# Kernel optimization log

Hardware: AMD Instinct MI355X
Metric: run time of the kernel (lower is better)

## Reference

```python
import jax, jax.numpy as jnp
import numpy as np

HID = 64
NUM_LAYERS = 4
IN_DIM = 1
OUT_DIM = 1
LN_EPS = 1e-5


def setup_inputs() -> dict:
    key = jax.random.key(0)
    ks = jax.random.split(key, 2 * NUM_LAYERS + 5)
    B, S = 1024, 512
    inp = {"x": jax.random.normal(ks[0], (B, S, IN_DIM), dtype=jnp.float32)}
    # per-layer gate weights, stored as [in+H, 4H] (x @ W + b, equivalent to torch Linear)
    for l in range(NUM_LAYERS):
        in_dim = IN_DIM if l == 0 else HID
        fan_in = in_dim + HID
        bound = 1.0 / np.sqrt(fan_in)
        inp[f"W{l}"] = jax.random.uniform(ks[1 + 2 * l], (fan_in, 4 * HID), jnp.float32, -bound, bound)
        inp[f"b{l}"] = jax.random.uniform(ks[2 + 2 * l], (4 * HID,), jnp.float32, -bound, bound)
    inp["ln_g"] = jnp.ones((HID,), jnp.float32)
    inp["ln_b"] = jnp.zeros((HID,), jnp.float32)
    bo = 1.0 / np.sqrt(HID)
    inp["Wout"] = jax.random.uniform(ks[-2], (HID, OUT_DIM), jnp.float32, -bo, bo)
    inp["bout"] = jax.random.uniform(ks[-1], (OUT_DIM,), jnp.float32, -bo, bo)
    return inp


def _lstm_forward(x, Ws, bs):
    B = x.shape[0]
    h0 = tuple(jnp.zeros((B, HID), x.dtype) for _ in range(NUM_LAYERS))
    c0 = tuple(jnp.zeros((B, HID), x.dtype) for _ in range(NUM_LAYERS))

    def step(carry, xt):
        h, c = carry
        inp = xt
        new_h, new_c = [], []
        for l in range(NUM_LAYERS):
            z = jnp.concatenate([inp, h[l]], axis=-1) @ Ws[l] + bs[l]  # [B, 4H]
            i, f, g, o = jnp.split(z, 4, axis=-1)
            i = jax.nn.sigmoid(i)
            f = jax.nn.sigmoid(f)
            g = jnp.tanh(g)
            o = jax.nn.sigmoid(o)
            c_new = f * c[l] + i * g
            h_new = o * jnp.tanh(c_new)
            new_h.append(h_new)
            new_c.append(c_new)
            inp = h_new
        return (tuple(new_h), tuple(new_c)), new_h[-1]

    xs = jnp.swapaxes(x, 0, 1)  # [S, B, in]
    _, outs = jax.lax.scan(step, (h0, c0), xs)
    return jnp.swapaxes(outs, 0, 1)  # [B, S, H]


def reference(x, W0, b0, W1, b1, W2, b2, W3, b3, ln_g, ln_b, Wout, bout):
    Ws = (W0, W1, W2, W3)
    bs = (b0, b1, b2, b3)
    out = _lstm_forward(x, Ws, bs)  # [B, S, H]
    mu = jnp.mean(out, axis=-1, keepdims=True)
    var = jnp.mean(jnp.square(out - mu), axis=-1, keepdims=True)
    normed = (out - mu) * jax.lax.rsqrt(var + LN_EPS) * ln_g + ln_b
    return normed @ Wout + bout  # [B, S, 1]
```

## Files before the change

### kernel.cpp

```cpp
#include <hip/hip_runtime.h>

#define SEQ   512
#define NTHR  1024
#define NBLK  256

typedef _Float16 f16x8 __attribute__((ext_vector_type(8)));
typedef float    f32x4 __attribute__((ext_vector_type(4)));

#define MFMA(a, b, c) __builtin_amdgcn_mfma_f32_16x16x32_f16((a), (b), (c), 0, 0, 0)

__device__ __forceinline__ float sig_(float x) {
    return __builtin_amdgcn_rcpf(1.0f + __builtin_amdgcn_exp2f(x * -1.4426950408889634f));
}
__device__ __forceinline__ float tanh_(float x) {
    return fmaf(2.0f, __builtin_amdgcn_rcpf(1.0f + __builtin_amdgcn_exp2f(x * -2.8853900817779268f)), -1.0f);
}

__global__ __launch_bounds__(NTHR, 4) void lstm4_pipe16b(
    const float* __restrict__ x,
    const float* __restrict__ W0, const float* __restrict__ B0,
    const float* __restrict__ W1, const float* __restrict__ B1,
    const float* __restrict__ W2, const float* __restrict__ B2,
    const float* __restrict__ W3, const float* __restrict__ B3,
    const float* __restrict__ ln_g, const float* __restrict__ ln_b,
    const float* __restrict__ Wout, const float* __restrict__ bout,
    float* __restrict__ out)
{
    __shared__ __align__(16) _Float16 hbuf[2][4][4][64];
    __shared__ float xall[4][SEQ];
    __shared__ float part[16][4][4][3];
    __shared__ float sconst[2];

    const int tid  = threadIdx.x;
    const int lane = tid & 63;
    const int w    = tid >> 6;
    const int ell  = w >> 2;
    const int om   = w & 3;
    const int lam  = lane >> 4;
    const int bc   = lane & 15;
    const int br   = bc & 3;
    const int k    = bc >> 2;
    const int bb   = blockIdx.x;

    for (int i = tid; i < 4 * SEQ; i += NTHR)
        xall[i >> 9][i & 511] = x[bb * 4 * SEQ + i];
    for (int i = tid; i < 2 * 4 * 4 * 64; i += NTHR)
        ((_Float16*)hbuf)[i] = (_Float16)0.0f;

    if (tid < 64) {
        float a = ln_g[tid] * Wout[tid];
        float b = ln_b[tid] * Wout[tid];
#pragma unroll
        for (int off = 32; off > 0; off >>= 1) {
            a += __shfl_xor(a, off, 64);
            b += __shfl_xor(b, off, 64);
        }
        if (tid == 0) { sconst[0] = a; sconst[1] = b; }
    }

    const float* Wp = (ell == 0) ? W0 : (ell == 1) ? W1 : (ell == 2) ? W2 : W3;
    const float* Bp = (ell == 0) ? B0 : (ell == 1) ? B1 : (ell == 2) ? B2 : B3;

    f16x8 wf[4][4];
    f32x4 biasv[4];
#pragma unroll
    for (int i = 0; i < 4; ++i) {
        const int T  = om * 4 + i;
        const int cA = (bc & 3) * 64 + T * 4 + (bc >> 2);
        if (ell == 0) {
#pragma unroll
            for (int kt = 0; kt < 2; ++kt)
#pragma unroll
                for (int e = 0; e < 8; ++e)
                    wf[i][kt][e] = (_Float16)W0[(1 + kt * 32 + lam * 8 + e) * 256 + cA];
#pragma unroll
            for (int e = 0; e < 8; ++e) { wf[i][2][e] = (_Float16)0.0f; wf[i][3][e] = (_Float16)0.0f; }
            if (lam == 0) wf[i][2][0] = (_Float16)W0[cA];
        } else {
#pragma unroll
            for (int kt = 0; kt < 4; ++kt)
#pragma unroll
                for (int e = 0; e < 8; ++e)
                    wf[i][kt][e] = (_Float16)Wp[(kt * 32 + lam * 8 + e) * 256 + cA];
        }
#pragma unroll
        for (int r = 0; r < 4; ++r)
            biasv[i][r] = Bp[r * 64 + T * 4 + lam];
    }

    const int   mK  = (om * 4 + k) * 4 + lam;
    const float gwK = ln_g[mK] * Wout[mK];
    const int   wrK = br * 128 + (((mK >> 3) ^ br) * 16) + (mK & 7) * 2;

    const int a0 = br * 128 + ((lam)     ^ br) * 16;
    const int a1 = br * 128 + ((4 + lam) ^ br) * 16;

    const bool k1b = (bc & 4) != 0;
    const bool k2b = (bc & 8) != 0;

    float cstK = 0.0f;
    char* const hb = (char*)hbuf;

    __syncthreads();
    const float Sgw = sconst[0];
    const float Sbw = sconst[1] + bout[0];

    for (int tau = 0; tau < SEQ + 3; ++tau) {
        const char* bR = hb + (((tau + 1) & 1) ? 2048 : 0);
        char*       bW = hb + (((tau    ) & 1) ? 2048 : 0);
        const int  t      = tau - ell;
        const bool active = (t >= 0) && (t < SEQ);

        if (active) {
            f16x8 b0, b1, b2, b3;
            if (ell == 0) {
                b0 = *(const f16x8*)(bR + a0);
                b1 = *(const f16x8*)(bR + a1);
                f16x8 xf;
#pragma unroll
                for (int e = 0; e < 8; ++e) xf[e] = (_Float16)0.0f;
                if (lam == 0) xf[0] = (_Float16)xall[br][t];
                b2 = xf; b3 = xf;
            } else {
                const char* bIn   = bR + (ell - 1) * 512;
                const char* bSelf = bR + ell * 512;
                b0 = *(const f16x8*)(bIn + a0);
                b1 = *(const f16x8*)(bIn + a1);
                b2 = *(const f16x8*)(bSelf + a0);
                b3 = *(const f16x8*)(bSelf + a1);
            }

            f32x4 A0 = MFMA(wf[0][0], b0, biasv[0]);
            f32x4 A1 = MFMA(wf[1][0], b0, biasv[1]);
            f32x4 A2 = MFMA(wf[2][0], b0, biasv[2]);
            f32x4 A3 = MFMA(wf[3][0], b0, biasv[3]);
            A0 = MFMA(wf[0][1], b1, A0);  A1 = MFMA(wf[1][1], b1, A1);
            A2 = MFMA(wf[2][1], b1, A2);  A3 = MFMA(wf[3][1], b1, A3);
            A0 = MFMA(wf[0][2], b2, A0);  A1 = MFMA(wf[1][2], b2, A1);
            A2 = MFMA(wf[2][2], b2, A2);  A3 = MFMA(wf[3][2], b2, A3);
            A0 = MFMA(wf[0][3], b3, A0);  A1 = MFMA(wf[1][3], b3, A1);
            A2 = MFMA(wf[2][3], b3, A2);  A3 = MFMA(wf[3][3], b3, A3);

            const f32x4 s01 = k1b ? A1 : A0;
            const f32x4 s23 = k1b ? A3 : A2;
            const f32x4 aK  = k2b ? s23 : s01;

            const float gi = sig_(aK[0]);
            const float gf = sig_(aK[1]);
            const float gg = tanh_(aK[2]);
            const float go = sig_(aK[3]);
            cstK = fmaf(gf, cstK, gi * gg);
            const float hn = go * tanh_(cstK);
            *(_Float16*)(bW + ell * 512 + wrK) = (_Float16)hn;

            if (ell == 3) {
                float v1 = hn, v2 = hn * hn, v3 = hn * gwK;
                v1 += __shfl_xor(v1, 4, 64);  v2 += __shfl_xor(v2, 4, 64);  v3 += __shfl_xor(v3, 4, 64);
                v1 += __shfl_xor(v1, 8, 64);  v2 += __shfl_xor(v2, 8, 64);  v3 += __shfl_xor(v3, 8, 64);
                v1 += __shfl_xor(v1, 16, 64); v2 += __shfl_xor(v2, 16, 64); v3 += __shfl_xor(v3, 16, 64);
                v1 += __shfl_xor(v1, 32, 64); v2 += __shfl_xor(v2, 32, 64); v3 += __shfl_xor(v3, 32, 64);
                if (bc < 4) {
                    float* pp = &part[t & 15][om][bc][0];
                    pp[0] = v1; pp[1] = v2; pp[2] = v3;
                }
            }
        }
        __syncthreads();

        const int t3 = tau - 3;
        if (t3 >= 7 && (t3 & 7) == 7) {
            const int row = tid >> 4, sub = tid & 15;
            if (row < 32) {
                const int sl = row >> 2, b = row & 3;
                const int slot = (t3 - 7 + sl) & 15;
                float u1 = part[slot][sub & 3][b][0];
                float u2 = part[slot][sub & 3][b][1];
                float u3 = part[slot][sub & 3][b][2];
                u1 += __shfl_xor(u1, 1, 64); u2 += __shfl_xor(u2, 1, 64); u3 += __shfl_xor(u3, 1, 64);
                u1 += __shfl_xor(u1, 2, 64); u2 += __shfl_xor(u2, 2, 64); u3 += __shfl_xor(u3, 2, 64);
                if (sub == 0) {
                    const float mu = u1 * (1.0f / 64.0f);
                    float var = fmaf(u2, 1.0f / 64.0f, -mu * mu);
                    var = fmaxf(var, 0.0f);
                    const float rs = rsqrtf(var + 1e-5f);
                    out[(bb * 4 + b) * SEQ + (t3 - 7) + sl] = fmaf(rs, fmaf(-mu, Sgw, u3), Sbw);
                }
            }
        }
    }
}

extern "C" void kernel_launch(void* const* d_in, const int* in_sizes, int n_in,
                              void* d_out, int out_size, void* d_ws, size_t ws_size,
                              hipStream_t stream)
{
    const float* x    = (const float*)d_in[0];
    const float* W0   = (const float*)d_in[1];
    const float* B0   = (const float*)d_in[2];
    const float* W1   = (const float*)d_in[3];
    const float* B1   = (const float*)d_in[4];
    const float* W2   = (const float*)d_in[5];
    const float* B2   = (const float*)d_in[6];
    const float* W3   = (const float*)d_in[7];
    const float* B3   = (const float*)d_in[8];
    const float* ln_g = (const float*)d_in[9];
    const float* ln_b = (const float*)d_in[10];
    const float* Wout = (const float*)d_in[11];
    const float* bout = (const float*)d_in[12];
    float* out = (float*)d_out;

    lstm4_pipe16b<<<NBLK, NTHR, 0, stream>>>(x, W0, B0, W1, B1, W2, B2, W3, B3,
                                             ln_g, ln_b, Wout, bout, out);
}
```

Measured before the change: 560.6 us.

## Stagger MFMA and gate phases across layer pairs with two barriers per step

Each iteration is split into two half-phases separated by barriers. Even layers run their MFMA in the first half while odd layers run gate activations, and the roles swap in the second half, so matrix and transcendental work from different wavefronts overlap on the CU. The final combine step is moved onto layer-3 wavefronts inside the loop. Barrier count per step doubles and the schedule skew grows to 517 iterations, which risks added sync overhead.

```diff
diff --git a/kernel.cpp b/kernel.cpp
--- a/kernel.cpp
+++ b/kernel.cpp
@@ -16,7 +16,84 @@
     return fmaf(2.0f, __builtin_amdgcn_rcpf(1.0f + __builtin_amdgcn_exp2f(x * -2.8853900817779268f)), -1.0f);
 }
 
-__global__ __launch_bounds__(NTHR, 4) void lstm4_pipe16b(
+
+#define MFMA_PHASE(T)                                                          \
+    {                                                                          \
+        const int pS = (((T) & 1) ^ 1) << 11;                                  \
+        f16x8 b0, b1, b2, b3;                                                  \
+        if (ell == 0) {                                                        \
+            b0 = *(const f16x8*)(hb + pS + sfA0);                              \
+            b1 = *(const f16x8*)(hb + pS + sfA1);                              \
+            if (lam == 0) xf[0] = (_Float16)xrow[T];                           \
+            b2 = xf; b3 = xf;                                                  \
+        } else {                                                               \
+            const int pI = ((T) & 1) << 11;                                    \
+            b0 = *(const f16x8*)(hb + pI + inA0);                              \
+            b1 = *(const f16x8*)(hb + pI + inA1);                              \
+            b2 = *(const f16x8*)(hb + pS + sfA0);                              \
+            b3 = *(const f16x8*)(hb + pS + sfA1);                              \
+        }                                                                      \
+        A0 = MFMA(wf[0][0], b0, biasv[0]);                                     \
+        A1 = MFMA(wf[1][0], b0, biasv[1]);                                     \
+        A2 = MFMA(wf[2][0], b0, biasv[2]);                                     \
+        A3 = MFMA(wf[3][0], b0, biasv[3]);                                     \
+        A0 = MFMA(wf[0][1], b1, A0);  A1 = MFMA(wf[1][1], b1, A1);             \
+        A2 = MFMA(wf[2][1], b1, A2);  A3 = MFMA(wf[3][1], b1, A3);             \
+        A0 = MFMA(wf[0][2], b2, A0);  A1 = MFMA(wf[1][2], b2, A1);             \
+        A2 = MFMA(wf[2][2], b2, A2);  A3 = MFMA(wf[3][2], b2, A3);             \
+        A0 = MFMA(wf[0][3], b3, A0);  A1 = MFMA(wf[1][3], b3, A1);             \
+        A2 = MFMA(wf[2][3], b3, A2);  A3 = MFMA(wf[3][3], b3, A3);             \
+    }
+
+#define GATES_PHASE(T)                                                         \
+    {                                                                          \
+        const f32x4 s01 = k1b ? A1 : A0;                                       \
+        const f32x4 s23 = k1b ? A3 : A2;                                       \
+        const f32x4 aK  = k2b ? s23 : s01;                                     \
+        const float gi = sig_(aK[0]);                                          \
+        const float gf = sig_(aK[1]);                                          \
+        const float gg = tanh_(aK[2]);                                         \
+        const float go = sig_(aK[3]);                                          \
+        cstK = fmaf(gf, cstK, gi * gg);                                        \
+        const float hn = go * tanh_(cstK);                                     \
+        *(_Float16*)(hb + (((T) & 1) << 11) + wrKS) = (_Float16)hn;            \
+        if (ell == 3) {                                                        \
+            float v1 = hn, v2 = hn * hn, v3 = hn * gwK;                        \
+            v1 += __shfl_xor(v1, 4, 64);  v2 += __shfl_xor(v2, 4, 64);  v3 += __shfl_xor(v3, 4, 64);  \
+            v1 += __shfl_xor(v1, 8, 64);  v2 += __shfl_xor(v2, 8, 64);  v3 += __shfl_xor(v3, 8, 64);  \
+            v1 += __shfl_xor(v1, 16, 64); v2 += __shfl_xor(v2, 16, 64); v3 += __shfl_xor(v3, 16, 64); \
+            v1 += __shfl_xor(v1, 32, 64); v2 += __shfl_xor(v2, 32, 64); v3 += __shfl_xor(v3, 32, 64); \
+            if (bc < 4) {                                                      \
+                float* pp = &part[(T) & 15][om][bc][0];                        \
+                pp[0] = v1; pp[1] = v2; pp[2] = v3;                            \
+            }                                                                  \
+        }                                                                      \
+    }
+
+#define COMBINE3(TG)                                                           \
+    {                                                                          \
+        const int sl = om * 2 + (lane >> 5);                                   \
+        const int b  = (lane >> 3) & 3;                                        \
+        const int j  = lane & 7;                                               \
+        const int slot = ((TG) - 7 + sl) & 15;                                 \
+        float u1 = 0.f, u2 = 0.f, u3 = 0.f;                                    \
+        if (j < 4) {                                                           \
+            u1 = part[slot][j][b][0];                                          \
+            u2 = part[slot][j][b][1];                                          \
+            u3 = part[slot][j][b][2];                                          \
+        }                                                                      \
+        u1 += __shfl_xor(u1, 1, 64); u2 += __shfl_xor(u2, 1, 64); u3 += __shfl_xor(u3, 1, 64); \
+        u1 += __shfl_xor(u1, 2, 64); u2 += __shfl_xor(u2, 2, 64); u3 += __shfl_xor(u3, 2, 64); \
+        if (j == 0) {                                                          \
+            const float mu = u1 * (1.0f / 64.0f);                              \
+            float var = fmaf(u2, 1.0f / 64.0f, -mu * mu);                      \
+            var = fmaxf(var, 0.0f);                                            \
+            const float rs = rsqrtf(var + 1e-5f);                              \
+            out[(bb * 4 + b) * SEQ + ((TG) - 7) + sl] = fmaf(rs, fmaf(-mu, Sgw, u3), Sbw); \
+        }                                                                      \
+    }
+
+__global__ __launch_bounds__(NTHR, 4) void lstm4_stag(
     const float* __restrict__ x,
     const float* __restrict__ W0, const float* __restrict__ B0,
     const float* __restrict__ W1, const float* __restrict__ B1,
@@ -39,7 +116,7 @@
     const int lam  = lane >> 4;
     const int bc   = lane & 15;
     const int br   = bc & 3;
-    const int k    = bc >> 2;
+    const int kq   = bc >> 2;
     const int bb   = blockIdx.x;
 
     for (int i = tid; i < 4 * SEQ; i += NTHR)
@@ -88,105 +165,58 @@
             biasv[i][r] = Bp[r * 64 + T * 4 + lam];
     }
 
-    const int   mK  = (om * 4 + k) * 4 + lam;
+    const int   mK  = (om * 4 + kq) * 4 + lam;
     const float gwK = ln_g[mK] * Wout[mK];
     const int   wrK = br * 128 + (((mK >> 3) ^ br) * 16) + (mK & 7) * 2;
 
     const int a0 = br * 128 + ((lam)     ^ br) * 16;
     const int a1 = br * 128 + ((4 + lam) ^ br) * 16;
 
+    const int inA0 = (ell == 0) ? a0 : (ell - 1) * 512 + a0;
+    const int inA1 = (ell == 0) ? a1 : (ell - 1) * 512 + a1;
+    const int sfA0 = ell * 512 + a0;
+    const int sfA1 = ell * 512 + a1;
+    const int wrKS = ell * 512 + wrK;
+    const float* const xrow = &xall[br][0];
+
     const bool k1b = (bc & 4) != 0;
     const bool k2b = (bc & 8) != 0;
+    const bool evenL = ((ell & 1) == 0);
+    const int  skM   = (ell == 0) ? 0 : (ell == 1) ? 1 : (ell == 2) ? 3 : 4;
+
+    f16x8 xf;
+#pragma unroll
+    for (int e = 0; e < 8; ++e) xf[e] = (_Float16)0.0f;
 
     float cstK = 0.0f;
+    f32x4 A0 = {}, A1 = {}, A2 = {}, A3 = {};
     char* const hb = (char*)hbuf;
 
     __syncthreads();
     const float Sgw = sconst[0];
     const float Sbw = sconst[1] + bout[0];
 
-    for (int tau = 0; tau < SEQ + 3; ++tau) {
-        const char* bR = hb + (((tau + 1) & 1) ? 2048 : 0);
-        char*       bW = hb + (((tau    ) & 1) ? 2048 : 0);
-        const int  t      = tau - ell;
-        const bool active = (t >= 0) && (t < SEQ);
-
-        if (active) {
-            f16x8 b0, b1, b2, b3;
-            if (ell == 0) {
-                b0 = *(const f16x8*)(bR + a0);
-                b1 = *(const f16x8*)(bR + a1);
-                f16x8 xf;
-#pragma unroll
-                for (int e = 0; e < 8; ++e) xf[e] = (_Float16)0.0f;
-                if (lam == 0) xf[0] = (_Float16)xall[br][t];
-                b2 = xf; b3 = xf;
-            } else {
-                const char* bIn   = bR + (ell - 1) * 512;
-                const char* bSelf = bR + ell * 512;
-                b0 = *(const f16x8*)(bIn + a0);
-                b1 = *(const f16x8*)(bIn + a1);
-                b2 = *(const f16x8*)(bSelf + a0);
-                b3 = *(const f16x8*)(bSelf + a1);
-            }
-
-            f32x4 A0 = MFMA(wf[0][0], b0, biasv[0]);
-            f32x4 A1 = MFMA(wf[1][0], b0, biasv[1]);
-            f32x4 A2 = MFMA(wf[2][0], b0, biasv[2]);
-            f32x4 A3 = MFMA(wf[3][0], b0, biasv[3]);
-            A0 = MFMA(wf[0][1], b1, A0);  A1 = MFMA(wf[1][1], b1, A1);
-            A2 = MFMA(wf[2][1], b1, A2);  A3 = MFMA(wf[3][1], b1, A3);
-            A0 = MFMA(wf[0][2], b2, A0);  A1 = MFMA(wf[1][2], b2, A1);
-            A2 = MFMA(wf[2][2], b2, A2);  A3 = MFMA(wf[3][2], b2, A3);
-            A0 = MFMA(wf[0][3], b3, A0);  A1 = MFMA(wf[1][3], b3, A1);
-            A2 = MFMA(wf[2][3], b3, A2);  A3 = MFMA(wf[3][3], b3, A3);
-
-            const f32x4 s01 = k1b ? A1 : A0;
-            const f32x4 s23 = k1b ? A3 : A2;
-            const f32x4 aK  = k2b ? s23 : s01;
-
-            const float gi = sig_(aK[0]);
-            const float gf = sig_(aK[1]);
-            const float gg = tanh_(aK[2]);
-            const float go = sig_(aK[3]);
-            cstK = fmaf(gf, cstK, gi * gg);
-            const float hn = go * tanh_(cstK);
-            *(_Float16*)(bW + ell * 512 + wrK) = (_Float16)hn;
-
-            if (ell == 3) {
-                float v1 = hn, v2 = hn * hn, v3 = hn * gwK;
-                v1 += __shfl_xor(v1, 4, 64);  v2 += __shfl_xor(v2, 4, 64);  v3 += __shfl_xor(v3, 4, 64);
-                v1 += __shfl_xor(v1, 8, 64);  v2 += __shfl_xor(v2, 8, 64);  v3 += __shfl_xor(v3, 8, 64);
-                v1 += __shfl_xor(v1, 16, 64); v2 += __shfl_xor(v2, 16, 64); v3 += __shfl_xor(v3, 16, 64);
-                v1 += __shfl_xor(v1, 32, 64); v2 += __shfl_xor(v2, 32, 64); v3 += __shfl_xor(v3, 32, 64);
-                if (bc < 4) {
-                    float* pp = &part[t & 15][om][bc][0];
-                    pp[0] = v1; pp[1] = v2; pp[2] = v3;
-                }
-            }
+    for (int k = 0; k <= 516; ++k) {
+        const int tM = k - skM;
+
+        if (evenL) {
+            if ((unsigned)tM < (unsigned)SEQ) MFMA_PHASE(tM)
+        } else {
+            const int tG = tM - 1;
+            if ((unsigned)tG < (unsigned)SEQ) GATES_PHASE(tG)
         }
         __syncthreads();
 
-        const int t3 = tau - 3;
-        if (t3 >= 7 && (t3 & 7) == 7) {
-            const int row = tid >> 4, sub = tid & 15;
-            if (row < 32) {
-                const int sl = row >> 2, b = row & 3;
-                const int slot = (t3 - 7 + sl) & 15;
-                float u1 = part[slot][sub & 3][b][0];
-                float u2 = part[slot][sub & 3][b][1];
-                float u3 = part[slot][sub & 3][b][2];
-                u1 += __shfl_xor(u1, 1, 64); u2 += __shfl_xor(u2, 1, 64); u3 += __shfl_xor(u3, 1, 64);
-                u1 += __shfl_xor(u1, 2, 64); u2 += __shfl_xor(u2, 2, 64); u3 += __shfl_xor(u3, 2, 64);
-                if (sub == 0) {
-                    const float mu = u1 * (1.0f / 64.0f);
-                    float var = fmaf(u2, 1.0f / 64.0f, -mu * mu);
-                    var = fmaxf(var, 0.0f);
-                    const float rs = rsqrtf(var + 1e-5f);
-                    out[(bb * 4 + b) * SEQ + (t3 - 7) + sl] = fmaf(rs, fmaf(-mu, Sgw, u3), Sbw);
-                }
-            }
-        }
+        if (evenL) {
+            if ((unsigned)tM < (unsigned)SEQ) GATES_PHASE(tM)
+        } else {
+            if ((unsigned)tM < (unsigned)SEQ) MFMA_PHASE(tM)
+        }
+        if (ell == 3) {
+            const int tg3 = k - 5;
+            if (tg3 >= 7 && (tg3 & 7) == 7) COMBINE3(tg3)
+        }
+        __syncthreads();
     }
 }
 
@@ -209,6 +239,6 @@
     const float* bout = (const float*)d_in[12];
     float* out = (float*)d_out;
 
-    lstm4_pipe16b<<<NBLK, NTHR, 0, stream>>>(x, W0, B0, W1, B1, W2, B2, W3, B3,
-                                             ln_g, ln_b, Wout, bout, out);
-}
+    lstm4_stag<<<NBLK, NTHR, 0, stream>>>(x, W0, B0, W1, B1, W2, B2, W3, B3,
+                                          ln_g, ln_b, Wout, bout, out);
+}
```

Result: slower. 654.4 us (+16.7%).
